# Performance work log

Hardware: AMD Instinct MI355X
Metric: run time of the kernel (lower is better)

Reference implementation:

```python
import jax, jax.numpy as jnp
import numpy as np
import math

# IPA hyperparameters (AlphaFold2 / ProtSeed defaults)
H, C, PQ, PV = 12, 16, 4, 8
CS, CZ = 384, 128
INF, EPS = 1e5, 1e-8
CAT = H * (CZ + C + 4 * PV)  # 2112


def setup_inputs() -> dict:
    key = jax.random.key(0)
    ks = jax.random.split(key, 20)
    B, N = 1, 512
    s = jax.random.normal(ks[0], (B, N, CS), jnp.float32)
    z = jax.random.normal(ks[1], (B, N, N, CZ), jnp.float32)
    # valid rotation matrices via QR of random gaussians
    rot = jnp.linalg.qr(jax.random.normal(ks[2], (B, N, 3, 3), jnp.float32))[0]
    trans = jax.random.normal(ks[3], (B, N, 3), jnp.float32)
    mask = jnp.ones((B, N), jnp.float32)
    sc = 0.02
    params = {
        'w_q': jax.random.normal(ks[4], (CS, H * C), jnp.float32) * sc,
        'b_q': jnp.zeros((H * C,), jnp.float32),
        'w_kv': jax.random.normal(ks[5], (CS, 2 * H * C), jnp.float32) * sc,
        'b_kv': jnp.zeros((2 * H * C,), jnp.float32),
        'w_qp': jax.random.normal(ks[6], (CS, H * PQ * 3), jnp.float32) * sc,
        'b_qp': jnp.zeros((H * PQ * 3,), jnp.float32),
        'w_kvp': jax.random.normal(ks[7], (CS, H * (PQ + PV) * 3), jnp.float32) * sc,
        'b_kvp': jnp.zeros((H * (PQ + PV) * 3,), jnp.float32),
        'w_b': jax.random.normal(ks[8], (CZ, H), jnp.float32) * sc,
        'b_b': jnp.zeros((H,), jnp.float32),
        'head_weights': jnp.full((H,), 0.5414, jnp.float32),  # softplus^-1(1)
        'w_out': jax.random.normal(ks[9], (CAT, CS), jnp.float32) * sc,
        'b_out': jnp.zeros((CS,), jnp.float32),
    }
    return {'s': s, 'z': z, 'rot': rot, 'trans': trans, 'mask': mask, **params}


def reference(s, z, rot, trans, mask, w_q, b_q, w_kv, b_kv, w_qp, b_qp,
              w_kvp, b_kvp, w_b, b_b, head_weights, w_out, b_out):
    B, N, _ = s.shape
    w_c = math.sqrt(1.0 / (3 * C))
    w_l = math.sqrt(1.0 / 3)
    w_p = math.sqrt(1.0 / (3 * (PQ * 9.0 / 2)))

    # scalar q/k/v: [B,N,H,C]
    q = (s @ w_q + b_q).reshape(B, N, H, C)
    kv = (s @ w_kv + b_kv).reshape(B, N, H, 2 * C)
    k, v = kv[..., :C], kv[..., C:]

    # point q/k/v in global frame. torch splits the projection into 3 chunks
    # (x,y,z) along the channel dim then stacks -> [B,N,H*P,3]
    def to_pts(w, b, p):
        pts = jnp.stack(jnp.split(s @ w + b, 3, axis=-1), axis=-1)  # [B,N,H*p,3]
        pts = jnp.einsum('bnij,bnpj->bnpi', rot, pts) + trans[:, :, None, :]
        return pts.reshape(B, N, H, p, 3)

    q_pts = to_pts(w_qp, b_qp, PQ)
    kv_pts = to_pts(w_kvp, b_kvp, PQ + PV)
    k_pts, v_pts = kv_pts[..., :PQ, :], kv_pts[..., PQ:, :]

    # pair bias [B,N,N,H]
    bias = z @ w_b + b_b

    # scalar attention logits [B,H,i,j]
    a = jnp.einsum('bihc,bjhc->bhij', q, k) * w_c
    a = a + w_l * jnp.transpose(bias, (0, 3, 1, 2))

    # point-distance term: [B,i,j,H,PQ]
    d2 = jnp.sum((q_pts[:, :, None] - k_pts[:, None]) ** 2, axis=-1)
    hw = jax.nn.softplus(head_weights) * w_p
    pt_att = -0.5 * jnp.sum(d2 * hw[None, None, None, :, None], axis=-1)  # [B,i,j,H]
    a = a + jnp.transpose(pt_att, (0, 3, 1, 2))

    sq_mask = INF * (mask[:, :, None] * mask[:, None, :] - 1.0)  # [B,i,j]
    a = jax.nn.softmax(a + sq_mask[:, None], axis=-1)  # [B,H,i,j]

    # scalar output [B,N,H*C]
    o = jnp.einsum('bhij,bjhc->bihc', a, v).reshape(B, N, H * C)

    # point output, mapped back to local frames: [B,i,H,PV,3]
    o_pt = jnp.einsum('bhij,bjhpx->bihpx', a, v_pts)
    o_pt = jnp.einsum('bnji,bnhpj->bnhpi', rot, o_pt - trans[:, :, None, None, :])
    o_pt_norm = jnp.sqrt(jnp.sum(o_pt ** 2, axis=-1) + EPS).reshape(B, N, H * PV)
    o_pt = o_pt.reshape(B, N, H * PV, 3)

    # pair output [B,N,H*CZ]
    o_pair = jnp.einsum('bhij,bijc->bihc', a, z).reshape(B, N, H * CZ)

    cat = jnp.concatenate(
        [o, o_pt[..., 0], o_pt[..., 1], o_pt[..., 2], o_pt_norm, o_pair], axis=-1)
    return cat @ w_out + b_out  # [B,N,C_s]
```

## Files before the change

### kernel.cpp

```cpp
#include <hip/hip_runtime.h>
#include <math.h>

#define NN 512
#define CSd 384
#define Hh 12
#define CATd 2112
#define KF_CHUNK 264
#define KF_SPLIT 8

__global__ void k_projgemm(const float* __restrict__ s,
                           const float* __restrict__ w_q, const float* __restrict__ b_q,
                           const float* __restrict__ w_kv, const float* __restrict__ b_kv,
                           const float* __restrict__ w_qp, const float* __restrict__ b_qp,
                           const float* __restrict__ w_kvp, const float* __restrict__ b_kvp,
                           float* __restrict__ proj)
{
  __shared__ float sT[384 * 40];
  const int t  = threadIdx.x;
  const int i0 = blockIdx.x * 32;
  const int c0 = blockIdx.y * 64;

  for (int u = t; u < 32 * 384; u += 256) {
    int row = u / 384, col = u % 384;
    sT[col * 40 + row] = s[(i0 + row) * CSd + col];
  }
  __syncthreads();

  const int c    = t & 63;
  const int rgrp = t >> 6;
  const int gc   = c0 + c;

  const float* wp;
  int stride;
  float bias;
  if (gc < 192)      { wp = w_q   + gc;         stride = 192; bias = b_q[gc]; }
  else if (gc < 576) { wp = w_kv  + (gc - 192); stride = 384; bias = b_kv[gc - 192]; }
  else if (gc < 720) { wp = w_qp  + (gc - 576); stride = 144; bias = b_qp[gc - 576]; }
  else               { wp = w_kvp + (gc - 720); stride = 432; bias = b_kvp[gc - 720]; }

  float acc[8];
#pragma unroll
  for (int j = 0; j < 8; j++) acc[j] = bias;

  const int r0 = rgrp * 8;
#pragma unroll 4
  for (int kk = 0; kk < 384; kk++) {
    float wv = *wp; wp += stride;
    const float4 a0 = *reinterpret_cast<const float4*>(&sT[kk * 40 + r0]);
    const float4 a1 = *reinterpret_cast<const float4*>(&sT[kk * 40 + r0 + 4]);
    acc[0] += a0.x * wv; acc[1] += a0.y * wv; acc[2] += a0.z * wv; acc[3] += a0.w * wv;
    acc[4] += a1.x * wv; acc[5] += a1.y * wv; acc[6] += a1.z * wv; acc[7] += a1.w * wv;
  }
#pragma unroll
  for (int j = 0; j < 8; j++)
    proj[(size_t)(i0 + r0 + j) * 1152 + gc] = acc[j];
}

__global__ void k_rot(const float* __restrict__ proj,
                      const float* __restrict__ rot, const float* __restrict__ trans,
                      float* __restrict__ q, float* __restrict__ kT, float* __restrict__ v,
                      float* __restrict__ qp, float* __restrict__ kpT, float* __restrict__ vp)
{
  __shared__ float ptsL[576];
  const int i = blockIdx.x, t = threadIdx.x;
  const float* pr = proj + (size_t)i * 1152;

  for (int u = t; u < 576; u += 256) ptsL[u] = pr[576 + u];

  for (int cI = t; cI < 576; cI += 256) {
    float pv = pr[cI];
    if (cI < 192) q[i * 192 + cI] = pv;
    else {
      int local = cI - 192, h = local >> 5, cc = local & 31;
      if (cc < 16) kT[(size_t)(h * 16 + cc) * NN + i] = pv;
      else         v[i * 192 + h * 16 + cc - 16] = pv;
    }
  }
  __syncthreads();

  for (int p = t; p < 192; p += 256) {
    float x, y, zz;
    if (p < 48) { x = ptsL[p]; y = ptsL[48 + p]; zz = ptsL[96 + p]; }
    else { int idx = p - 48; x = ptsL[144 + idx]; y = ptsL[288 + idx]; zz = ptsL[432 + idx]; }
    const float* Rm = rot + i * 9;
    const float* tr = trans + i * 3;
    float rx = Rm[0] * x + Rm[1] * y + Rm[2] * zz + tr[0];
    float ry = Rm[3] * x + Rm[4] * y + Rm[5] * zz + tr[1];
    float rz = Rm[6] * x + Rm[7] * y + Rm[8] * zz + tr[2];
    if (p < 48) {
      float* d = qp + ((size_t)i * 48 + p) * 3;
      d[0] = rx; d[1] = ry; d[2] = rz;
    } else {
      int idx = p - 48, h = idx / 12, pp = idx % 12;
      if (pp < 4) {
        size_t rbase = (size_t)((h * 4 + pp) * 3) * NN + i;
        kpT[rbase] = rx; kpT[rbase + NN] = ry; kpT[rbase + 2 * NN] = rz;
      } else {
        float* d = vp + ((size_t)i * 96 + h * 8 + pp - 4) * 3;
        d[0] = rx; d[1] = ry; d[2] = rz;
      }
    }
  }
}

__global__ void k_bias(const float* __restrict__ z, const float* __restrict__ w_b,
                       const float* __restrict__ b_b, const float* __restrict__ mask,
                       float* __restrict__ a)
{
  __shared__ float zL[64 * 132];
  __shared__ float wT[12 * 128];
  __shared__ float red[4][64][13];
  const int t = threadIdx.x;
  const int row0 = blockIdx.x * 64;
  const int i = row0 >> 9;
  const int j0 = row0 & 511;

  for (int u = t; u < 1536; u += 256) {
    int h = u >> 7, c = u & 127;
    wT[u] = w_b[c * 12 + h];
  }
  const float4* z4 = reinterpret_cast<const float4*>(z + (size_t)row0 * 128);
  for (int u = t; u < 64 * 32; u += 256) {
    int r = u >> 5, c4 = u & 31;
    *reinterpret_cast<float4*>(&zL[r * 132 + c4 * 4]) = z4[u];
  }
  __syncthreads();

  const int r = t & 63, cq = t >> 6;
  float4 zr[8];
#pragma unroll
  for (int i4 = 0; i4 < 8; i4++)
    zr[i4] = *reinterpret_cast<const float4*>(&zL[r * 132 + cq * 32 + i4 * 4]);

  float acc[12];
#pragma unroll
  for (int h = 0; h < 12; h++) {
    float sv = 0.f;
#pragma unroll
    for (int i4 = 0; i4 < 8; i4++) {
      const float4 w = *reinterpret_cast<const float4*>(&wT[h * 128 + cq * 32 + i4 * 4]);
      sv += zr[i4].x * w.x + zr[i4].y * w.y + zr[i4].z * w.z + zr[i4].w * w.w;
    }
    acc[h] = sv;
  }
#pragma unroll
  for (int h = 0; h < 12; h++) red[cq][r][h] = acc[h];
  __syncthreads();

  const int rr = t & 63, hg = t >> 6;
  const float mi = mask[i], mj = mask[j0 + rr];
  const float mterm = 100000.0f * (mi * mj - 1.0f);
  const float W_L = 0.57735026919f;
#pragma unroll
  for (int h = hg * 3; h < hg * 3 + 3; h++) {
    float sv = b_b[h] + red[0][rr][h] + red[1][rr][h] + red[2][rr][h] + red[3][rr][h];
    a[((size_t)h * NN + i) * NN + j0 + rr] = W_L * sv + mterm;
  }
}

__global__ void k_attn(const float* __restrict__ q, const float* __restrict__ kT,
                       const float* __restrict__ qp, const float* __restrict__ kpT,
                       const float* __restrict__ hws, float* __restrict__ a)
{
  const int i = blockIdx.x, h = blockIdx.y, t = threadIdx.x;
  __shared__ float qL[16], qpL[12];
  __shared__ float red[2][4];
  if (t < 16) qL[t] = q[i * 192 + h * 16 + t];
  else if (t >= 32 && t < 44) qpL[t - 32] = qp[(size_t)i * 144 + h * 12 + (t - 32)];
  __syncthreads();

  const float hwv = 0.13608276348f * log1pf(expf(hws[h]));
  const float W_C = 0.14433756730f;
  const size_t base = ((size_t)h * NN + i) * NN;
  const int j = t * 2;

  float2 lg = *reinterpret_cast<const float2*>(&a[base + j]);

  float dx = 0.f, dy = 0.f;
#pragma unroll
  for (int c = 0; c < 16; c++) {
    float2 kv = *reinterpret_cast<const float2*>(&kT[(size_t)((h << 4) + c) * NN + j]);
    dx += qL[c] * kv.x; dy += qL[c] * kv.y;
  }
  float s2x = 0.f, s2y = 0.f;
#pragma unroll
  for (int pc = 0; pc < 12; pc++) {
    float2 kv = *reinterpret_cast<const float2*>(&kpT[(size_t)(h * 12 + pc) * NN + j]);
    float qv = qpL[pc];
    float ddx = qv - kv.x, ddy = qv - kv.y;
    s2x += ddx * ddx; s2y += ddy * ddy;
  }
  lg.x += W_C * dx - 0.5f * hwv * s2x;
  lg.y += W_C * dy - 0.5f * hwv * s2y;

  float m = fmaxf(lg.x, lg.y);
  for (int o = 1; o < 64; o <<= 1) m = fmaxf(m, __shfl_xor(m, o));
  if ((t & 63) == 0) red[0][t >> 6] = m;
  __syncthreads();
  m = fmaxf(fmaxf(red[0][0], red[0][1]), fmaxf(red[0][2], red[0][3]));
  float e0 = expf(lg.x - m), e1 = expf(lg.y - m);
  float sm = e0 + e1;
  for (int o = 1; o < 64; o <<= 1) sm += __shfl_xor(sm, o);
  if ((t & 63) == 0) red[1][t >> 6] = sm;
  __syncthreads();
  float inv = 1.0f / (red[1][0] + red[1][1] + red[1][2] + red[1][3]);
  float2 res = make_float2(e0 * inv, e1 * inv);
  *reinterpret_cast<float2*>(&a[base + j]) = res;
}

__global__ void k_out(const float* __restrict__ a, const float* __restrict__ v,
                      const float* __restrict__ vp, const float* __restrict__ z,
                      const float* __restrict__ rot, const float* __restrict__ trans,
                      float* __restrict__ cat)
{
  __shared__ float aL[12][513];
  __shared__ float optL[12][8][3];
  __shared__ float redp[4][12][129];
  const int i = blockIdx.x, t = threadIdx.x;
  for (int u = t; u < 12 * 512; u += 512)
    aL[u >> 9][u & 511] = a[((size_t)(u >> 9) * NN + i) * NN + (u & 511)];
  __syncthreads();

  {
    const int c = t & 127, jq = t >> 7;
    float pa[12];
#pragma unroll
    for (int h = 0; h < 12; h++) pa[h] = 0.f;
    const float* zr = z + (size_t)i * 65536 + c;
    const int jend = jq * 128 + 128;
    for (int j = jq * 128; j < jend; j++) {
      float zv = zr[(size_t)j * 128];
#pragma unroll
      for (int h = 0; h < 12; h++) pa[h] += aL[h][j] * zv;
    }
#pragma unroll
    for (int h = 0; h < 12; h++) redp[jq][h][c] = pa[h];
  }
  __syncthreads();

  if (t < 192) {
    float acc = 0.f;
    const int h = t >> 4;
    for (int j = 0; j < 512; j++) acc += aL[h][j] * v[(size_t)j * 192 + t];
    cat[(size_t)i * CATd + t] = acc;
  } else if (t < 480) {
    int u = t - 192, h = u / 24;
    float acc = 0.f;
    for (int j = 0; j < 512; j++) acc += aL[h][j] * vp[(size_t)j * 288 + u];
    int pc = u % 24;
    optL[h][pc / 3][pc % 3] = acc;
  }
  __syncthreads();

  if (t < 96) {
    int h = t >> 3, p = t & 7;
    const float* Rm = rot + i * 9;
    const float* tr = trans + i * 3;
    float ox = optL[h][p][0] - tr[0];
    float oy = optL[h][p][1] - tr[1];
    float oz = optL[h][p][2] - tr[2];
    float rx = Rm[0] * ox + Rm[3] * oy + Rm[6] * oz;
    float ry = Rm[1] * ox + Rm[4] * oy + Rm[7] * oz;
    float rz = Rm[2] * ox + Rm[5] * oy + Rm[8] * oz;
    float nrm = sqrtf(rx * rx + ry * ry + rz * rz + 1e-8f);
    size_t b = (size_t)i * CATd;
    cat[b + 192 + t] = rx; cat[b + 288 + t] = ry;
    cat[b + 384 + t] = rz; cat[b + 480 + t] = nrm;
  }

#pragma unroll
  for (int kph = 0; kph < 3; kph++) {
    int e = t + kph * 512;
    int h = e >> 7, c = e & 127;
    float sv = redp[0][h][c] + redp[1][h][c] + redp[2][h][c] + redp[3][h][c];
    cat[(size_t)i * CATd + 576 + e] = sv;
  }
}

__global__ void k_final(const float* __restrict__ cat, const float* __restrict__ w_out,
                        float* __restrict__ part)
{
  __shared__ float sT[KF_CHUNK * 36];
  const int t  = threadIdx.x;
  const int i0 = blockIdx.x * 32;
  const int c0 = blockIdx.y * 64;
  const int k0 = blockIdx.z * KF_CHUNK;

  for (int u = t; u < 32 * KF_CHUNK; u += 256) {
    int row = u / KF_CHUNK, kk = u % KF_CHUNK;
    sT[kk * 36 + row] = cat[(size_t)(i0 + row) * CATd + k0 + kk];
  }
  __syncthreads();

  const int c    = t & 63;
  const int rgrp = t >> 6;
  const int r0   = rgrp * 8;
  const int gc   = c0 + c;

  float acc[8];
#pragma unroll
  for (int j = 0; j < 8; j++) acc[j] = 0.f;

  const float* wp = w_out + (size_t)k0 * 384 + gc;
#pragma unroll 4
  for (int kk = 0; kk < KF_CHUNK; kk++) {
    float wv = wp[(size_t)kk * 384];
    const float4 a0 = *reinterpret_cast<const float4*>(&sT[kk * 36 + r0]);
    const float4 a1 = *reinterpret_cast<const float4*>(&sT[kk * 36 + r0 + 4]);
    acc[0] += a0.x * wv; acc[1] += a0.y * wv; acc[2] += a0.z * wv; acc[3] += a0.w * wv;
    acc[4] += a1.x * wv; acc[5] += a1.y * wv; acc[6] += a1.z * wv; acc[7] += a1.w * wv;
  }

  float* pb = part + (size_t)blockIdx.z * NN * 384;
#pragma unroll
  for (int j = 0; j < 8; j++)
    pb[(size_t)(i0 + r0 + j) * 384 + gc] = acc[j];
}

__global__ void k_reduce(const float* __restrict__ part, const float* __restrict__ b_out,
                         float* __restrict__ out)
{
  const int idx = blockIdx.x * 256 + threadIdx.x;
  const int c = idx % 384;
  float acc = b_out[c];
#pragma unroll
  for (int ks = 0; ks < KF_SPLIT; ks++)
    acc += part[(size_t)ks * NN * 384 + idx];
  out[idx] = acc;
}

extern "C" void kernel_launch(void* const* d_in, const int* in_sizes, int n_in,
                              void* d_out, int out_size, void* d_ws, size_t ws_size,
                              hipStream_t stream) {
  const float* s      = (const float*)d_in[0];
  const float* z      = (const float*)d_in[1];
  const float* rot    = (const float*)d_in[2];
  const float* trans  = (const float*)d_in[3];
  const float* mask   = (const float*)d_in[4];
  const float* w_q    = (const float*)d_in[5];
  const float* b_q    = (const float*)d_in[6];
  const float* w_kv   = (const float*)d_in[7];
  const float* b_kv   = (const float*)d_in[8];
  const float* w_qp   = (const float*)d_in[9];
  const float* b_qp   = (const float*)d_in[10];
  const float* w_kvp  = (const float*)d_in[11];
  const float* b_kvp  = (const float*)d_in[12];
  const float* w_b    = (const float*)d_in[13];
  const float* b_b    = (const float*)d_in[14];
  const float* hws    = (const float*)d_in[15];
  const float* w_out  = (const float*)d_in[16];
  const float* b_out  = (const float*)d_in[17];
  float* out = (float*)d_out;

  float* ws  = (float*)d_ws;
  float* q   = ws;
  float* kT  = q  + 98304;
  float* v   = kT + 98304;
  float* qp  = v  + 98304;
  float* kpT = qp + 73728;
  float* vp  = kpT + 73728;
  float* a   = vp + 147456;
  float* cat = a  + 3145728;
  float* proj = a;
  float* part = a;

  k_projgemm<<<dim3(16, 18), 256, 0, stream>>>(s, w_q, b_q, w_kv, b_kv,
                                               w_qp, b_qp, w_kvp, b_kvp, proj);
  k_rot<<<512, 256, 0, stream>>>(proj, rot, trans, q, kT, v, qp, kpT, vp);
  k_bias<<<4096, 256, 0, stream>>>(z, w_b, b_b, mask, a);
  k_attn<<<dim3(512, 12), 256, 0, stream>>>(q, kT, qp, kpT, hws, a);
  k_out<<<512, 512, 0, stream>>>(a, v, vp, z, rot, trans, cat);
  k_final<<<dim3(16, 6, KF_SPLIT), 256, 0, stream>>>(cat, w_out, part);
  k_reduce<<<768, 256, 0, stream>>>(part, b_out, out);
}
```

Baseline: 199.8 us.

## Fuse attention logits into bias kernel and softmax into output kernel

Removes the separate k_attn kernel. The scalar and point logit terms are now computed inside k_bias, and the row softmax is done in k_out on the shared-memory copy of the attention row. This saves one full read and write pass over the 12x512x512 logits tensor and one launch. k_out is also restructured: it uses a padded shared layout, a register-blocked pair-output loop (12 heads x 8 channels per thread with float4 z loads and shuffle reductions), and a merged v/v_pts buffer for the scalar and point outputs. The cost is much heavier register pressure in k_out (96 accumulators under launch_bounds 512,2) and scattered kT/kpT reads in k_bias.

```diff
diff --git a/kernel.cpp b/kernel.cpp
--- a/kernel.cpp
+++ b/kernel.cpp
@@ -3,10 +3,16 @@
 
 #define NN 512
 #define CSd 384
-#define Hh 12
 #define CATd 2112
 #define KF_CHUNK 264
 #define KF_SPLIT 8
+
+__device__ __forceinline__ int aidx(int h, int j) {
+  return h * 544 + ((j >> 6) * 68) + (j & 63);
+}
+__device__ __forceinline__ float f4c(const float4& v, int k) {
+  return k == 0 ? v.x : (k == 1 ? v.y : (k == 2 ? v.z : v.w));
+}
 
 __global__ void k_projgemm(const float* __restrict__ s,
                            const float* __restrict__ w_q, const float* __restrict__ b_q,
@@ -58,8 +64,8 @@
 
 __global__ void k_rot(const float* __restrict__ proj,
                       const float* __restrict__ rot, const float* __restrict__ trans,
-                      float* __restrict__ q, float* __restrict__ kT, float* __restrict__ v,
-                      float* __restrict__ qp, float* __restrict__ kpT, float* __restrict__ vp)
+                      float* __restrict__ q, float* __restrict__ kT, float* __restrict__ vcat,
+                      float* __restrict__ qp, float* __restrict__ kpT)
 {
   __shared__ float ptsL[576];
   const int i = blockIdx.x, t = threadIdx.x;
@@ -73,7 +79,7 @@
     else {
       int local = cI - 192, h = local >> 5, cc = local & 31;
       if (cc < 16) kT[(size_t)(h * 16 + cc) * NN + i] = pv;
-      else         v[i * 192 + h * 16 + cc - 16] = pv;
+      else         vcat[(size_t)i * 480 + h * 16 + (cc - 16)] = pv;
     }
   }
   __syncthreads();
@@ -96,8 +102,8 @@
         size_t rbase = (size_t)((h * 4 + pp) * 3) * NN + i;
         kpT[rbase] = rx; kpT[rbase + NN] = ry; kpT[rbase + 2 * NN] = rz;
       } else {
-        float* d = vp + ((size_t)i * 96 + h * 8 + pp - 4) * 3;
-        d[0] = rx; d[1] = ry; d[2] = rz;
+        size_t rbase = (size_t)i * 480 + 192 + (h * 8 + pp - 4) * 3;
+        vcat[rbase] = rx; vcat[rbase + 1] = ry; vcat[rbase + 2] = rz;
       }
     }
   }
@@ -105,11 +111,15 @@
 
 __global__ void k_bias(const float* __restrict__ z, const float* __restrict__ w_b,
                        const float* __restrict__ b_b, const float* __restrict__ mask,
+                       const float* __restrict__ q, const float* __restrict__ kT,
+                       const float* __restrict__ qp, const float* __restrict__ kpT,
+                       const float* __restrict__ hws,
                        float* __restrict__ a)
 {
   __shared__ float zL[64 * 132];
   __shared__ float wT[12 * 128];
   __shared__ float red[4][64][13];
+  __shared__ float qL[192], qpL[144], hwL[12];
   const int t = threadIdx.x;
   const int row0 = blockIdx.x * 64;
   const int i = row0 >> 9;
@@ -124,141 +134,228 @@
     int r = u >> 5, c4 = u & 31;
     *reinterpret_cast<float4*>(&zL[r * 132 + c4 * 4]) = z4[u];
   }
-  __syncthreads();
-
-  const int r = t & 63, cq = t >> 6;
-  float4 zr[8];
-#pragma unroll
-  for (int i4 = 0; i4 < 8; i4++)
-    zr[i4] = *reinterpret_cast<const float4*>(&zL[r * 132 + cq * 32 + i4 * 4]);
-
-  float acc[12];
-#pragma unroll
-  for (int h = 0; h < 12; h++) {
-    float sv = 0.f;
-#pragma unroll
-    for (int i4 = 0; i4 < 8; i4++) {
-      const float4 w = *reinterpret_cast<const float4*>(&wT[h * 128 + cq * 32 + i4 * 4]);
-      sv += zr[i4].x * w.x + zr[i4].y * w.y + zr[i4].z * w.z + zr[i4].w * w.w;
-    }
-    acc[h] = sv;
-  }
-#pragma unroll
-  for (int h = 0; h < 12; h++) red[cq][r][h] = acc[h];
-  __syncthreads();
-
-  const int rr = t & 63, hg = t >> 6;
-  const float mi = mask[i], mj = mask[j0 + rr];
+  for (int u = t; u < 192; u += 256) qL[u] = q[i * 192 + u];
+  for (int u = t; u < 144; u += 256) qpL[u] = qp[(size_t)i * 144 + u];
+  for (int u = t; u < 12; u += 256) hwL[u] = 0.13608276348f * log1pf(expf(hws[u]));
+  __syncthreads();
+
+  {
+    const int r = t & 63, cq = t >> 6;
+    float4 zr[8];
+#pragma unroll
+    for (int i4 = 0; i4 < 8; i4++)
+      zr[i4] = *reinterpret_cast<const float4*>(&zL[r * 132 + cq * 32 + i4 * 4]);
+#pragma unroll
+    for (int h = 0; h < 12; h++) {
+      float sv = 0.f;
+#pragma unroll
+      for (int i4 = 0; i4 < 8; i4++) {
+        const float4 w = *reinterpret_cast<const float4*>(&wT[h * 128 + cq * 32 + i4 * 4]);
+        sv += zr[i4].x * w.x + zr[i4].y * w.y + zr[i4].z * w.z + zr[i4].w * w.w;
+      }
+      red[cq][r][h] = sv;
+    }
+  }
+  __syncthreads();
+
+  const int r = t & 63, hg = t >> 6;
+  const float mi = mask[i], mj = mask[j0 + r];
   const float mterm = 100000.0f * (mi * mj - 1.0f);
   const float W_L = 0.57735026919f;
-#pragma unroll
+  const float W_C = 0.14433756730f;
   for (int h = hg * 3; h < hg * 3 + 3; h++) {
-    float sv = b_b[h] + red[0][rr][h] + red[1][rr][h] + red[2][rr][h] + red[3][rr][h];
-    a[((size_t)h * NN + i) * NN + j0 + rr] = W_L * sv + mterm;
-  }
-}
-
-__global__ void k_attn(const float* __restrict__ q, const float* __restrict__ kT,
-                       const float* __restrict__ qp, const float* __restrict__ kpT,
-                       const float* __restrict__ hws, float* __restrict__ a)
-{
-  const int i = blockIdx.x, h = blockIdx.y, t = threadIdx.x;
-  __shared__ float qL[16], qpL[12];
-  __shared__ float red[2][4];
-  if (t < 16) qL[t] = q[i * 192 + h * 16 + t];
-  else if (t >= 32 && t < 44) qpL[t - 32] = qp[(size_t)i * 144 + h * 12 + (t - 32)];
-  __syncthreads();
-
-  const float hwv = 0.13608276348f * log1pf(expf(hws[h]));
-  const float W_C = 0.14433756730f;
-  const size_t base = ((size_t)h * NN + i) * NN;
-  const int j = t * 2;
-
-  float2 lg = *reinterpret_cast<const float2*>(&a[base + j]);
-
-  float dx = 0.f, dy = 0.f;
-#pragma unroll
-  for (int c = 0; c < 16; c++) {
-    float2 kv = *reinterpret_cast<const float2*>(&kT[(size_t)((h << 4) + c) * NN + j]);
-    dx += qL[c] * kv.x; dy += qL[c] * kv.y;
-  }
-  float s2x = 0.f, s2y = 0.f;
-#pragma unroll
-  for (int pc = 0; pc < 12; pc++) {
-    float2 kv = *reinterpret_cast<const float2*>(&kpT[(size_t)(h * 12 + pc) * NN + j]);
-    float qv = qpL[pc];
-    float ddx = qv - kv.x, ddy = qv - kv.y;
-    s2x += ddx * ddx; s2y += ddy * ddy;
-  }
-  lg.x += W_C * dx - 0.5f * hwv * s2x;
-  lg.y += W_C * dy - 0.5f * hwv * s2y;
-
-  float m = fmaxf(lg.x, lg.y);
-  for (int o = 1; o < 64; o <<= 1) m = fmaxf(m, __shfl_xor(m, o));
-  if ((t & 63) == 0) red[0][t >> 6] = m;
-  __syncthreads();
-  m = fmaxf(fmaxf(red[0][0], red[0][1]), fmaxf(red[0][2], red[0][3]));
-  float e0 = expf(lg.x - m), e1 = expf(lg.y - m);
-  float sm = e0 + e1;
-  for (int o = 1; o < 64; o <<= 1) sm += __shfl_xor(sm, o);
-  if ((t & 63) == 0) red[1][t >> 6] = sm;
-  __syncthreads();
-  float inv = 1.0f / (red[1][0] + red[1][1] + red[1][2] + red[1][3]);
-  float2 res = make_float2(e0 * inv, e1 * inv);
-  *reinterpret_cast<float2*>(&a[base + j]) = res;
-}
-
-__global__ void k_out(const float* __restrict__ a, const float* __restrict__ v,
-                      const float* __restrict__ vp, const float* __restrict__ z,
-                      const float* __restrict__ rot, const float* __restrict__ trans,
-                      float* __restrict__ cat)
-{
-  __shared__ float aL[12][513];
-  __shared__ float optL[12][8][3];
-  __shared__ float redp[4][12][129];
+    float sv = b_b[h] + red[0][r][h] + red[1][r][h] + red[2][r][h] + red[3][r][h];
+    float dot = 0.f;
+#pragma unroll
+    for (int c = 0; c < 16; c++)
+      dot += qL[h * 16 + c] * kT[(size_t)(h * 16 + c) * NN + j0 + r];
+    float d2 = 0.f;
+#pragma unroll
+    for (int pc = 0; pc < 12; pc++) {
+      float kv = kpT[(size_t)(h * 12 + pc) * NN + j0 + r];
+      float dd = qpL[h * 12 + pc] - kv;
+      d2 += dd * dd;
+    }
+    a[((size_t)h * NN + i) * NN + j0 + r] = W_L * sv + mterm + W_C * dot - 0.5f * hwL[h] * d2;
+  }
+}
+
+__global__ void __launch_bounds__(512, 2)
+k_out(const float* __restrict__ a, const float* __restrict__ vcat,
+      const float* __restrict__ z,
+      const float* __restrict__ rot, const float* __restrict__ trans,
+      float* __restrict__ cat)
+{
+  __shared__ float aL[12 * 544];
+  __shared__ float redp[8][16][56];
+  __shared__ float optF[288];
+  float* red2 = &redp[0][0][0];
+
   const int i = blockIdx.x, t = threadIdx.x;
-  for (int u = t; u < 12 * 512; u += 512)
-    aL[u >> 9][u & 511] = a[((size_t)(u >> 9) * NN + i) * NN + (u & 511)];
+
+  for (int u = t; u < 12 * 512; u += 512) {
+    int h = u >> 9, j = u & 511;
+    aL[aidx(h, j)] = a[((size_t)h * NN + i) * NN + j];
+  }
   __syncthreads();
 
   {
-    const int c = t & 127, jq = t >> 7;
-    float pa[12];
-#pragma unroll
-    for (int h = 0; h < 12; h++) pa[h] = 0.f;
-    const float* zr = z + (size_t)i * 65536 + c;
-    const int jend = jq * 128 + 128;
-    for (int j = jq * 128; j < jend; j++) {
-      float zv = zr[(size_t)j * 128];
-#pragma unroll
-      for (int h = 0; h < 12; h++) pa[h] += aL[h][j] * zv;
-    }
-#pragma unroll
-    for (int h = 0; h < 12; h++) redp[jq][h][c] = pa[h];
-  }
-  __syncthreads();
-
-  if (t < 192) {
-    float acc = 0.f;
-    const int h = t >> 4;
-    for (int j = 0; j < 512; j++) acc += aL[h][j] * v[(size_t)j * 192 + t];
-    cat[(size_t)i * CATd + t] = acc;
-  } else if (t < 480) {
-    int u = t - 192, h = u / 24;
-    float acc = 0.f;
-    for (int j = 0; j < 512; j++) acc += aL[h][j] * vp[(size_t)j * 288 + u];
-    int pc = u % 24;
-    optL[h][pc / 3][pc % 3] = acc;
+    const int wv = t >> 6, l = t & 63;
+    for (int h = wv; h < 12; h += 8) {
+      const int j0 = l * 8;
+      float4 x0 = *reinterpret_cast<const float4*>(&aL[aidx(h, j0)]);
+      float4 x1 = *reinterpret_cast<const float4*>(&aL[aidx(h, j0 + 4)]);
+      float m8 = fmaxf(fmaxf(fmaxf(x0.x, x0.y), fmaxf(x0.z, x0.w)),
+                       fmaxf(fmaxf(x1.x, x1.y), fmaxf(x1.z, x1.w)));
+      for (int o = 1; o < 64; o <<= 1) m8 = fmaxf(m8, __shfl_xor(m8, o));
+      x0.x = expf(x0.x - m8); x0.y = expf(x0.y - m8);
+      x0.z = expf(x0.z - m8); x0.w = expf(x0.w - m8);
+      x1.x = expf(x1.x - m8); x1.y = expf(x1.y - m8);
+      x1.z = expf(x1.z - m8); x1.w = expf(x1.w - m8);
+      float s8 = x0.x + x0.y + x0.z + x0.w + x1.x + x1.y + x1.z + x1.w;
+      for (int o = 1; o < 64; o <<= 1) s8 += __shfl_xor(s8, o);
+      float inv = 1.0f / s8;
+      x0.x *= inv; x0.y *= inv; x0.z *= inv; x0.w *= inv;
+      x1.x *= inv; x1.y *= inv; x1.z *= inv; x1.w *= inv;
+      *reinterpret_cast<float4*>(&aL[aidx(h, j0)]) = x0;
+      *reinterpret_cast<float4*>(&aL[aidx(h, j0 + 4)]) = x1;
+    }
+  }
+  __syncthreads();
+
+  const int cg = t & 15;
+  const int jq = (t >> 4) & 3;
+  const int wv = t >> 6;
+  float acc1[12][8];
+#pragma unroll
+  for (int h = 0; h < 12; h++)
+#pragma unroll
+    for (int c = 0; c < 8; c++) acc1[h][c] = 0.f;
+
+  {
+    const int c8 = cg * 8;
+    const int jb = wv * 64 + jq * 16;
+    const float* zb = z + (size_t)i * 65536 + c8;
+    for (int ch = 0; ch < 4; ch++) {
+      const int j0c = jb + ch * 4;
+      float4 p4[12];
+#pragma unroll
+      for (int h = 0; h < 12; h++)
+        p4[h] = *reinterpret_cast<const float4*>(&aL[aidx(h, j0c)]);
+#pragma unroll
+      for (int jj = 0; jj < 4; jj++) {
+        const float4 za = *reinterpret_cast<const float4*>(&zb[(size_t)(j0c + jj) * 128]);
+        const float4 zc = *reinterpret_cast<const float4*>(&zb[(size_t)(j0c + jj) * 128 + 4]);
+#pragma unroll
+        for (int h = 0; h < 12; h++) {
+          const float pv = f4c(p4[h], jj);
+          acc1[h][0] += pv * za.x; acc1[h][1] += pv * za.y;
+          acc1[h][2] += pv * za.z; acc1[h][3] += pv * za.w;
+          acc1[h][4] += pv * zc.x; acc1[h][5] += pv * zc.y;
+          acc1[h][6] += pv * zc.z; acc1[h][7] += pv * zc.w;
+        }
+      }
+    }
+#pragma unroll
+    for (int h = 0; h < 12; h++)
+#pragma unroll
+      for (int c = 0; c < 8; c++) {
+        float v2 = acc1[h][c];
+        v2 += __shfl_xor(v2, 16);
+        v2 += __shfl_xor(v2, 32);
+        acc1[h][c] = v2;
+      }
+  }
+
+  if (jq == 0) {
+#pragma unroll
+    for (int h = 0; h < 6; h++) {
+      *reinterpret_cast<float4*>(&redp[wv][cg][h * 8]) =
+        make_float4(acc1[h][0], acc1[h][1], acc1[h][2], acc1[h][3]);
+      *reinterpret_cast<float4*>(&redp[wv][cg][h * 8 + 4]) =
+        make_float4(acc1[h][4], acc1[h][5], acc1[h][6], acc1[h][7]);
+    }
+  }
+  __syncthreads();
+  for (int e = t; e < 768; e += 512) {
+    int h = e >> 7, c = e & 127;
+    float sv = 0.f;
+#pragma unroll
+    for (int w2 = 0; w2 < 8; w2++) sv += redp[w2][c >> 3][h * 8 + (c & 7)];
+    cat[(size_t)i * CATd + 576 + e] = sv;
+  }
+  __syncthreads();
+
+  if (jq == 0) {
+#pragma unroll
+    for (int h = 0; h < 6; h++) {
+      *reinterpret_cast<float4*>(&redp[wv][cg][h * 8]) =
+        make_float4(acc1[6 + h][0], acc1[6 + h][1], acc1[6 + h][2], acc1[6 + h][3]);
+      *reinterpret_cast<float4*>(&redp[wv][cg][h * 8 + 4]) =
+        make_float4(acc1[6 + h][4], acc1[6 + h][5], acc1[6 + h][6], acc1[6 + h][7]);
+    }
+  }
+  __syncthreads();
+  for (int e = t; e < 768; e += 512) {
+    int h = e >> 7, c = e & 127;
+    float sv = 0.f;
+#pragma unroll
+    for (int w2 = 0; w2 < 8; w2++) sv += redp[w2][c >> 3][h * 8 + (c & 7)];
+    cat[(size_t)i * CATd + 576 + 768 + e] = sv;
+  }
+  __syncthreads();
+
+  const int oc = t & 63, jw = t >> 6;
+  const int h2 = oc / 5, c5 = oc - h2 * 5;
+  const int c8b = c5 * 8;
+  float acc2[8];
+#pragma unroll
+  for (int c = 0; c < 8; c++) acc2[c] = 0.f;
+
+  if (oc < 60) {
+    const int vbase = (c8b < 16) ? (h2 * 16 + c8b) : (192 + h2 * 24 + (c8b - 16));
+    for (int ch = 0; ch < 16; ch++) {
+      const int j0c = jw * 64 + ch * 4;
+      const float4 p4 = *reinterpret_cast<const float4*>(&aL[aidx(h2, j0c)]);
+#pragma unroll
+      for (int jj = 0; jj < 4; jj++) {
+        const float* vr = &vcat[(size_t)(j0c + jj) * 480 + vbase];
+        const float4 va = *reinterpret_cast<const float4*>(vr);
+        const float4 vb = *reinterpret_cast<const float4*>(vr + 4);
+        const float pv = f4c(p4, jj);
+        acc2[0] += pv * va.x; acc2[1] += pv * va.y;
+        acc2[2] += pv * va.z; acc2[3] += pv * va.w;
+        acc2[4] += pv * vb.x; acc2[5] += pv * vb.y;
+        acc2[6] += pv * vb.z; acc2[7] += pv * vb.w;
+      }
+    }
+  }
+  if (oc < 60) {
+    *reinterpret_cast<float4*>(&red2[((size_t)jw * 64 + oc) * 8]) =
+      make_float4(acc2[0], acc2[1], acc2[2], acc2[3]);
+    *reinterpret_cast<float4*>(&red2[((size_t)jw * 64 + oc) * 8 + 4]) =
+      make_float4(acc2[4], acc2[5], acc2[6], acc2[7]);
+  }
+  __syncthreads();
+
+  for (int e = t; e < 480; e += 512) {
+    const int oc2 = e >> 3, cc = e & 7;
+    float sv = 0.f;
+#pragma unroll
+    for (int w2 = 0; w2 < 8; w2++) sv += red2[((size_t)w2 * 64 + oc2) * 8 + cc];
+    const int hh = e / 40, c40 = e - hh * 40;
+    if (c40 < 16) cat[(size_t)i * CATd + hh * 16 + c40] = sv;
+    else optF[hh * 24 + (c40 - 16)] = sv;
   }
   __syncthreads();
 
   if (t < 96) {
-    int h = t >> 3, p = t & 7;
+    const int h = t >> 3, p = t & 7;
     const float* Rm = rot + i * 9;
     const float* tr = trans + i * 3;
-    float ox = optL[h][p][0] - tr[0];
-    float oy = optL[h][p][1] - tr[1];
-    float oz = optL[h][p][2] - tr[2];
+    float ox = optF[h * 24 + p * 3 + 0] - tr[0];
+    float oy = optF[h * 24 + p * 3 + 1] - tr[1];
+    float oz = optF[h * 24 + p * 3 + 2] - tr[2];
     float rx = Rm[0] * ox + Rm[3] * oy + Rm[6] * oz;
     float ry = Rm[1] * ox + Rm[4] * oy + Rm[7] * oz;
     float rz = Rm[2] * ox + Rm[5] * oy + Rm[8] * oz;
@@ -266,14 +363,6 @@
     size_t b = (size_t)i * CATd;
     cat[b + 192 + t] = rx; cat[b + 288 + t] = ry;
     cat[b + 384 + t] = rz; cat[b + 480 + t] = nrm;
-  }
-
-#pragma unroll
-  for (int kph = 0; kph < 3; kph++) {
-    int e = t + kph * 512;
-    int h = e >> 7, c = e & 127;
-    float sv = redp[0][h][c] + redp[1][h][c] + redp[2][h][c] + redp[3][h][c];
-    cat[(size_t)i * CATd + 576 + e] = sv;
   }
 }
 
@@ -352,24 +441,22 @@
   const float* b_out  = (const float*)d_in[17];
   float* out = (float*)d_out;
 
-  float* ws  = (float*)d_ws;
-  float* q   = ws;
-  float* kT  = q  + 98304;
-  float* v   = kT + 98304;
-  float* qp  = v  + 98304;
-  float* kpT = qp + 73728;
-  float* vp  = kpT + 73728;
-  float* a   = vp + 147456;
-  float* cat = a  + 3145728;
+  float* ws   = (float*)d_ws;
+  float* q    = ws;
+  float* kT   = q    + 98304;
+  float* vcat = kT   + 98304;
+  float* qp   = vcat + 245760;
+  float* kpT  = qp   + 73728;
+  float* a    = kpT  + 73728;
+  float* cat  = a    + 3145728;
   float* proj = a;
   float* part = a;
 
   k_projgemm<<<dim3(16, 18), 256, 0, stream>>>(s, w_q, b_q, w_kv, b_kv,
                                                w_qp, b_qp, w_kvp, b_kvp, proj);
-  k_rot<<<512, 256, 0, stream>>>(proj, rot, trans, q, kT, v, qp, kpT, vp);
-  k_bias<<<4096, 256, 0, stream>>>(z, w_b, b_b, mask, a);
-  k_attn<<<dim3(512, 12), 256, 0, stream>>>(q, kT, qp, kpT, hws, a);
-  k_out<<<512, 512, 0, stream>>>(a, v, vp, z, rot, trans, cat);
+  k_rot<<<512, 256, 0, stream>>>(proj, rot, trans, q, kT, vcat, qp, kpT);
+  k_bias<<<4096, 256, 0, stream>>>(z, w_b, b_b, mask, q, kT, qp, kpT, hws, a);
+  k_out<<<512, 512, 0, stream>>>(a, vcat, z, rot, trans, cat);
   k_final<<<dim3(16, 6, KF_SPLIT), 256, 0, stream>>>(cat, w_out, part);
   k_reduce<<<768, 256, 0, stream>>>(part, b_out, out);
 }
```

Measured after the change: 252.0 us. +26.1%, slower.
